# Kernel tuning notes

Measured on AMD Instinct MI355X. Metric: run time of the kernel, lower is better.

The kernel has to match this reference:

```python
import jax, jax.numpy as jnp
import numpy as np

DIM_H = 128
HEADS = 8
HEAD_DIM = DIM_H // HEADS
N_NODES = 40000
N_EDGES = 640000
BN_EPS = 1e-5


def setup_inputs() -> dict:
    key = jax.random.key(0)
    ks = jax.random.split(key, 16)
    s = 0.05
    x = jax.random.normal(ks[0], (N_NODES, DIM_H), dtype=jnp.float32)
    edge_index = jax.random.randint(ks[1], (2, N_EDGES), 0, N_NODES, dtype=jnp.int64)
    p = lambda k, shp: jax.random.normal(k, shp, dtype=jnp.float32) * s
    return {
        "x": x,
        "edge_index": edge_index,
        "Wk": p(ks[2], (DIM_H, DIM_H)), "bk": p(ks[3], (DIM_H,)),
        "Wv": p(ks[4], (DIM_H, DIM_H)), "bv": p(ks[5], (DIM_H,)),
        "Wo": p(ks[6], (DIM_H, DIM_H)), "bo": p(ks[7], (DIM_H,)),
        "bn1_g": jnp.ones((DIM_H,), jnp.float32), "bn1_b": jnp.zeros((DIM_H,), jnp.float32),
        "W1": p(ks[8], (2 * DIM_H, DIM_H)), "b1": p(ks[9], (2 * DIM_H,)),
        "W2": p(ks[10], (DIM_H, 2 * DIM_H)), "b2": p(ks[11], (DIM_H,)),
        "bn2_g": jnp.ones((DIM_H,), jnp.float32), "bn2_b": jnp.zeros((DIM_H,), jnp.float32),
    }


def _batchnorm(h, gamma, beta):
    # BatchNorm1d in training mode: per-feature batch mean / biased var over nodes
    mu = jnp.mean(h, axis=0)
    var = jnp.mean((h - mu) ** 2, axis=0)
    return (h - mu) * jax.lax.rsqrt(var + BN_EPS) * gamma + beta


def _sparse_attn(x, edge_index, Wk, bk, Wv, bv, Wo, bo):
    N = x.shape[0]
    src, dst = edge_index[0], edge_index[1]
    K = (x @ Wk.T + bk).reshape(N, HEADS, HEAD_DIM)
    V = (x @ Wv.T + bv).reshape(N, HEADS, HEAD_DIM)
    Q = x.reshape(N, HEADS, HEAD_DIM)  # query is raw h (no projection)
    # per-edge scores [E, H]
    scores = jnp.sum(K[src] * Q[dst], axis=-1) / np.sqrt(HEAD_DIM).astype(np.float32)
    # segment softmax over destination nodes (pyg_softmax)
    m = jax.ops.segment_max(scores, dst, num_segments=N)
    e = jnp.exp(scores - m[dst])
    denom = jax.ops.segment_sum(e, dst, num_segments=N)
    attn = e / (denom[dst] + 1e-16)  # [E, H]
    messages = V[src] * attn[:, :, None]  # [E, H, D]
    out = jax.ops.segment_sum(messages, dst, num_segments=N)  # [N, H, D]
    return out.reshape(N, DIM_H) @ Wo.T + bo


def reference(x, edge_index, Wk, bk, Wv, bv, Wo, bo, bn1_g, bn1_b,
              W1, b1, W2, b2, bn2_g, bn2_b):
    h_attn = _sparse_attn(x, edge_index, Wk, bk, Wv, bv, Wo, bo)
    h = _batchnorm(x + h_attn, bn1_g, bn1_b)
    ff = jax.nn.relu(h @ W1.T + b1) @ W2.T + b2
    h = _batchnorm(h + ff, bn2_g, bn2_b)
    return h
```

## Files before the change

kernel.cpp:

```cpp
#include <hip/hip_runtime.h>

#define DIM 128
#define NSHARD 8

typedef __attribute__((ext_vector_type(2))) float f32x2;
typedef __attribute__((ext_vector_type(4))) _Float16 half4;
typedef __attribute__((ext_vector_type(8))) _Float16 half8;
typedef __attribute__((ext_vector_type(4))) float f32x4;

#define HP 136
#define UP 264

__device__ __forceinline__ unsigned char to_fp8(float v) {
  return (unsigned char)(__builtin_amdgcn_cvt_pk_fp8_f32(v, v, 0, false) & 0xff);
}

__global__ __launch_bounds__(256) void conv_wall(const float* __restrict__ Wk,
    const float* __restrict__ Wv, const float* __restrict__ Wo,
    const float* __restrict__ W1, const float* __restrict__ W2,
    _Float16* __restrict__ Wkh, _Float16* __restrict__ Wvh,
    _Float16* __restrict__ Woh, _Float16* __restrict__ W1h,
    _Float16* __restrict__ W2h, int* __restrict__ cnt, float* __restrict__ stats,
    int N) {
  int i = blockIdx.x * 256 + threadIdx.x;
  int nth = gridDim.x * 256;
  if (i < 16384) Wkh[i] = (_Float16)Wk[i];
  else if (i < 32768) Wvh[i - 16384] = (_Float16)Wv[i - 16384];
  else if (i < 49152) Woh[i - 32768] = (_Float16)Wo[i - 32768];
  else if (i < 81920) W1h[i - 49152] = (_Float16)W1[i - 49152];
  else if (i < 114688) W2h[i - 81920] = (_Float16)W2[i - 81920];
  for (int j = i; j < N * NSHARD; j += nth) cnt[j] = 0;
  if (i < 512) stats[i] = 0.f;
}

__global__ __launch_bounds__(256) void hist_rank(const int* __restrict__ ei,
    int* __restrict__ cnt, int* __restrict__ rank, int N, int E) {
  int e = blockIdx.x * 256 + threadIdx.x;
  if (e < E) rank[e] = atomicAdd(&cnt[(e & (NSHARD - 1)) * N + ei[E + e]], 1);
}

__global__ __launch_bounds__(256) void scanA(const int* __restrict__ cnt,
    int* __restrict__ rs, int* __restrict__ bsum, int N) {
  __shared__ int s[256];
  int t = threadIdx.x;
  int i = blockIdx.x * 256 + t;
  int v = 0;
  if (i < N)
#pragma unroll
    for (int sh = 0; sh < NSHARD; sh++) v += cnt[sh * N + i];
  s[t] = v;
  __syncthreads();
  for (int off = 1; off < 256; off <<= 1) {
    int add = (t >= off) ? s[t - off] : 0;
    __syncthreads();
    s[t] += add;
    __syncthreads();
  }
  if (i < N) rs[i] = s[t] - v;
  if (t == 255) bsum[blockIdx.x] = s[t];
}

__global__ __launch_bounds__(256) void scanBC(int* __restrict__ rs,
    const int* __restrict__ bsum, const int* __restrict__ cnt,
    int* __restrict__ rs_shard, int nblk, int N, int E) {
  __shared__ int s[256];
  __shared__ int ex[256];
  int t = threadIdx.x;
  int v = (t < nblk) ? bsum[t] : 0;
  s[t] = v;
  __syncthreads();
  for (int off = 1; off < 256; off <<= 1) {
    int add = (t >= off) ? s[t - off] : 0;
    __syncthreads();
    s[t] += add;
    __syncthreads();
  }
  ex[t] = s[t] - v;
  __syncthreads();
  int boff = ex[blockIdx.x];
  int i = blockIdx.x * 256 + t;
  if (i < N) {
    int b = rs[i] + boff;
    rs[i] = b;
#pragma unroll
    for (int sh = 0; sh < NSHARD; sh++) {
      rs_shard[sh * N + i] = b;
      b += cnt[sh * N + i];
    }
  }
  if (i == 0) rs[N] = E;
}

__global__ __launch_bounds__(256) void scatter_kv(const int* __restrict__ ei,
    const int* __restrict__ rs_shard, const int* __restrict__ rank,
    int* __restrict__ esrc, const float* __restrict__ x,
    const _Float16* __restrict__ Wkh, const float* __restrict__ bk,
    const _Float16* __restrict__ Wvh, const float* __restrict__ bv,
    unsigned char* __restrict__ KV8, int kvb, int N, int E) {
  __shared__ _Float16 xs[64 * HP];
  int tid = threadIdx.x;
  if ((int)blockIdx.x >= kvb) {
    int e = ((int)blockIdx.x - kvb) * 256 + tid;
    if (e < E)
      esrc[rs_shard[(e & (NSHARD - 1)) * N + ei[E + e]] + rank[e]] = ei[e];
    return;
  }
  int base = blockIdx.x * 64;
  int lane = tid & 63, w = tid >> 6;
  int l15 = lane & 15, quad = lane >> 4;

  for (int i = tid; i < 64 * 32; i += 256) {
    int m = i >> 5, c4 = i & 31;
    float4 tv = ((const float4*)x)[(size_t)(base + m) * 32 + c4];
    half4 hv;
    hv.x = (_Float16)tv.x; hv.y = (_Float16)tv.y;
    hv.z = (_Float16)tv.z; hv.w = (_Float16)tv.w;
    *(half4*)&xs[m * HP + c4 * 4] = hv;
  }
  __syncthreads();

  half8 afr[4][4];
#pragma unroll
  for (int mt = 0; mt < 4; mt++)
#pragma unroll
    for (int ks = 0; ks < 4; ks++)
      afr[mt][ks] = *(const half8*)&xs[(mt * 16 + l15) * HP + ks * 32 + quad * 8];

  const _Float16* W = (w < 2) ? Wkh : Wvh;
  const float* bias = (w < 2) ? bk : bv;
  int voff = (w < 2) ? 0 : 4;
  int c0 = (w & 1) * 64;

#pragma unroll
  for (int nt = 0; nt < 4; nt++) {
    int f = c0 + nt * 16 + l15;
    half8 bfr[4];
#pragma unroll
    for (int ks = 0; ks < 4; ks++)
      bfr[ks] = *(const half8*)&W[(size_t)f * 128 + ks * 32 + quad * 8];
    f32x4 acc[4];
#pragma unroll
    for (int mt = 0; mt < 4; mt++) acc[mt] = (f32x4){0.f, 0.f, 0.f, 0.f};
#pragma unroll
    for (int ks = 0; ks < 4; ks++)
#pragma unroll
      for (int mt = 0; mt < 4; mt++)
        acc[mt] = __builtin_amdgcn_mfma_f32_16x16x32_f16(afr[mt][ks], bfr[ks],
                                                          acc[mt], 0, 0, 0);
    float bb = bias[f];
    int fo = (f >> 2) * 8 + (f & 3) + voff;
#pragma unroll
    for (int mt = 0; mt < 4; mt++)
#pragma unroll
      for (int r = 0; r < 4; r++)
        KV8[(size_t)(base + mt * 16 + quad * 4 + r) * 256 + fo] =
            to_fp8(acc[mt][r] + bb);
  }
}

__global__ __launch_bounds__(256) void attn_agg(const unsigned char* __restrict__ KV8,
    const float* __restrict__ x, const int* __restrict__ rs,
    const int* __restrict__ esrc, _Float16* __restrict__ attn16, int N) {
  int wave = threadIdx.x >> 6, lane = threadIdx.x & 63;
  int n = blockIdx.x * 4 + wave;
  if (n >= N) return;
  int l = lane & 31, s = lane >> 5;
  float4 q = *(const float4*)&x[(size_t)n * DIM + 4 * l];
  int beg = rs[n], end = rs[n + 1];
  float a0 = 0.f, a1 = 0.f, a2 = 0.f, a3 = 0.f, dloc = 0.f;
  for (int e = beg + s; e < end; e += 8) {
    bool hh[4];
    int ss[4];
#pragma unroll
    for (int u = 0; u < 4; u++) hh[u] = (e + 2 * u) < end;
    ss[0] = esrc[e];
#pragma unroll
    for (int u = 1; u < 4; u++) ss[u] = hh[u] ? esrc[e + 2 * u] : ss[0];
    uint2 kv[4];
#pragma unroll
    for (int u = 0; u < 4; u++)
      kv[u] = *(const uint2*)&KV8[(size_t)ss[u] * 256 + 8 * l];
    float p[4];
#pragma unroll
    for (int u = 0; u < 4; u++) {
      f32x2 k01 = __builtin_amdgcn_cvt_pk_f32_fp8(kv[u].x, false);
      f32x2 k23 = __builtin_amdgcn_cvt_pk_f32_fp8(kv[u].x, true);
      p[u] = k01[0] * q.x + k01[1] * q.y + k23[0] * q.z + k23[1] * q.w;
    }
#pragma unroll
    for (int u = 0; u < 4; u++) p[u] += __shfl_xor(p[u], 1);
#pragma unroll
    for (int u = 0; u < 4; u++) p[u] += __shfl_xor(p[u], 2);
#pragma unroll
    for (int u = 0; u < 4; u++) {
      float ev = hh[u] ? __expf(p[u] * 0.25f) : 0.f;
      dloc += ev;
      f32x2 v01 = __builtin_amdgcn_cvt_pk_f32_fp8(kv[u].y, false);
      f32x2 v23 = __builtin_amdgcn_cvt_pk_f32_fp8(kv[u].y, true);
      a0 += ev * v01[0];
      a1 += ev * v01[1];
      a2 += ev * v23[0];
      a3 += ev * v23[1];
    }
  }
  dloc += __shfl_xor(dloc, 32);
  a0 += __shfl_xor(a0, 32);
  a1 += __shfl_xor(a1, 32);
  a2 += __shfl_xor(a2, 32);
  a3 += __shfl_xor(a3, 32);
  if (s == 0) {
    float inv = 1.0f / (dloc + 1e-16f);
    half4 o;
    o.x = (_Float16)(a0 * inv);
    o.y = (_Float16)(a1 * inv);
    o.z = (_Float16)(a2 * inv);
    o.w = (_Float16)(a3 * inv);
    *(half4*)&attn16[(size_t)n * DIM + 4 * l] = o;
  }
}

__global__ __launch_bounds__(256) void o_proj_mfma(const _Float16* __restrict__ attn16,
    const float* __restrict__ x, const _Float16* __restrict__ Woh,
    const float* __restrict__ bo, _Float16* __restrict__ t16,
    float* __restrict__ stats, int N) {
  __shared__ _Float16 as16[64 * HP];
  int tid = threadIdx.x;
  int base = blockIdx.x * 64;
  int lane = tid & 63, w = tid >> 6;
  int l15 = lane & 15, quad = lane >> 4;

  for (int i = tid; i < 64 * 16; i += 256) {
    int m = i >> 4, c8 = i & 15;
    *(half8*)&as16[m * HP + c8 * 8] =
        ((const half8*)attn16)[(size_t)(base + m) * 16 + c8];
  }
  __syncthreads();

  half8 afr[4][4];
#pragma unroll
  for (int mt = 0; mt < 4; mt++)
#pragma unroll
    for (int ks = 0; ks < 4; ks++)
      afr[mt][ks] = *(const half8*)&as16[(mt * 16 + l15) * HP + ks * 32 + quad * 8];

  int c0 = w * 32;
  f32x4 acc[4][2];
#pragma unroll
  for (int mt = 0; mt < 4; mt++)
#pragma unroll
    for (int nt = 0; nt < 2; nt++) acc[mt][nt] = (f32x4){0.f, 0.f, 0.f, 0.f};
#pragma unroll
  for (int ks = 0; ks < 4; ks++) {
    half8 b[2];
#pragma unroll
    for (int nt = 0; nt < 2; nt++)
      b[nt] = *(const half8*)&Woh[(size_t)(c0 + nt * 16 + l15) * 128 + ks * 32 +
                                  quad * 8];
#pragma unroll
    for (int mt = 0; mt < 4; mt++)
#pragma unroll
      for (int nt = 0; nt < 2; nt++)
        acc[mt][nt] =
            __builtin_amdgcn_mfma_f32_16x16x32_f16(afr[mt][ks], b[nt], acc[mt][nt], 0, 0, 0);
  }

#pragma unroll
  for (int nt = 0; nt < 2; nt++) {
    int f = c0 + nt * 16 + l15;
    float bb = bo[f];
    float s = 0.f, q = 0.f;
#pragma unroll
    for (int mt = 0; mt < 4; mt++) {
#pragma unroll
      for (int r = 0; r < 4; r++) {
        int row = mt * 16 + quad * 4 + r;
        float tv = acc[mt][nt][r] + bb + x[(size_t)(base + row) * DIM + f];
        t16[(size_t)(base + row) * DIM + f] = (_Float16)tv;
        s += tv;
        q += tv * tv;
      }
    }
    s += __shfl_xor(s, 16);
    s += __shfl_xor(s, 32);
    q += __shfl_xor(q, 16);
    q += __shfl_xor(q, 32);
    if (quad == 0) {
      atomicAdd(&stats[f], s);
      atomicAdd(&stats[128 + f], q);
    }
  }
}

__global__ __launch_bounds__(256) void ffn_mfma(const _Float16* __restrict__ t16,
    const float* __restrict__ stats1, const float* __restrict__ g1,
    const float* __restrict__ bb1, const _Float16* __restrict__ W1h,
    const float* __restrict__ b1, const _Float16* __restrict__ W2h,
    const float* __restrict__ b2, _Float16* __restrict__ z16,
    float* __restrict__ stats2, float invN, int N) {
  __shared__ _Float16 hs[64 * HP];
  __shared__ _Float16 us[64 * UP];
  __shared__ float cf[256];
  int tid = threadIdx.x;
  int base = blockIdx.x * 64;
  int lane = tid & 63, w = tid >> 6;
  int l15 = lane & 15, quad = lane >> 4;

  if (tid < 128) {
    float mu = stats1[tid] * invN;
    float var = stats1[128 + tid] * invN - mu * mu;
    float a = rsqrtf(var + 1e-5f) * g1[tid];
    cf[tid] = a;
    cf[128 + tid] = bb1[tid] - mu * a;
  }
  __syncthreads();

  for (int i = tid; i < 64 * 16; i += 256) {
    int m = i >> 4, c8 = i & 15;
    half8 tv = ((const half8*)t16)[(size_t)(base + m) * 16 + c8];
    half8 hv;
#pragma unroll
    for (int j = 0; j < 8; j++) {
      int f = c8 * 8 + j;
      hv[j] = (_Float16)((float)tv[j] * cf[f] + cf[128 + f]);
    }
    *(half8*)&hs[m * HP + c8 * 8] = hv;
  }
  __syncthreads();

  int n0 = w * 64;
  half8 afr[4][4];
#pragma unroll
  for (int mt = 0; mt < 4; mt++)
#pragma unroll
    for (int ks = 0; ks < 4; ks++)
      afr[mt][ks] = *(const half8*)&hs[(mt * 16 + l15) * HP + ks * 32 + quad * 8];

#pragma unroll
  for (int nt = 0; nt < 4; nt++) {
    int n = n0 + nt * 16 + l15;
    half8 bfr[4];
#pragma unroll
    for (int ks = 0; ks < 4; ks++)
      bfr[ks] = *(const half8*)&W1h[(size_t)n * 128 + ks * 32 + quad * 8];
    f32x4 acc[4];
#pragma unroll
    for (int mt = 0; mt < 4; mt++) acc[mt] = (f32x4){0.f, 0.f, 0.f, 0.f};
#pragma unroll
    for (int ks = 0; ks < 4; ks++)
#pragma unroll
      for (int mt = 0; mt < 4; mt++)
        acc[mt] = __builtin_amdgcn_mfma_f32_16x16x32_f16(afr[mt][ks], bfr[ks],
                                                          acc[mt], 0, 0, 0);
    float bias = b1[n];
#pragma unroll
    for (int mt = 0; mt < 4; mt++)
#pragma unroll
      for (int r = 0; r < 4; r++)
        us[(mt * 16 + quad * 4 + r) * UP + n] =
            (_Float16)fmaxf(acc[mt][r] + bias, 0.f);
  }
  __syncthreads();

  int n2 = w * 32;
  f32x4 acc2[4][2];
#pragma unroll
  for (int mt = 0; mt < 4; mt++)
#pragma unroll
    for (int nt = 0; nt < 2; nt++) acc2[mt][nt] = (f32x4){0.f, 0.f, 0.f, 0.f};
  for (int ks = 0; ks < 8; ks++) {
    half8 a[4], b[2];
#pragma unroll
    for (int mt = 0; mt < 4; mt++)
      a[mt] = *(const half8*)&us[(mt * 16 + l15) * UP + ks * 32 + quad * 8];
#pragma unroll
    for (int nt = 0; nt < 2; nt++)
      b[nt] = *(const half8*)&W2h[(size_t)(n2 + nt * 16 + l15) * 256 + ks * 32 +
                                  quad * 8];
#pragma unroll
    for (int mt = 0; mt < 4; mt++)
#pragma unroll
      for (int nt = 0; nt < 2; nt++)
        acc2[mt][nt] =
            __builtin_amdgcn_mfma_f32_16x16x32_f16(a[mt], b[nt], acc2[mt][nt], 0, 0, 0);
  }

#pragma unroll
  for (int nt = 0; nt < 2; nt++) {
    int f = n2 + nt * 16 + l15;
    float bz = b2[f];
    float s = 0.f, q = 0.f;
#pragma unroll
    for (int mt = 0; mt < 4; mt++) {
#pragma unroll
      for (int r = 0; r < 4; r++) {
        int row = mt * 16 + quad * 4 + r;
        float hv = (float)hs[row * HP + f];
        float zv = hv + acc2[mt][nt][r] + bz;
        z16[(size_t)(base + row) * DIM + f] = (_Float16)zv;
        s += zv;
        q += zv * zv;
      }
    }
    s += __shfl_xor(s, 16);
    s += __shfl_xor(s, 32);
    q += __shfl_xor(q, 16);
    q += __shfl_xor(q, 32);
    if (quad == 0) {
      atomicAdd(&stats2[f], s);
      atomicAdd(&stats2[128 + f], q);
    }
  }
}

__global__ __launch_bounds__(256) void final_apply(const _Float16* __restrict__ z16,
    const float* __restrict__ stats2, const float* __restrict__ g2,
    const float* __restrict__ bb2, float* __restrict__ out, float invN,
    int total8) {
  __shared__ float cf[256];
  int tid = threadIdx.x;
  if (tid < 128) {
    float mu = stats2[tid] * invN;
    float var = stats2[128 + tid] * invN - mu * mu;
    float a = rsqrtf(var + 1e-5f) * g2[tid];
    cf[tid] = a;
    cf[128 + tid] = bb2[tid] - mu * a;
  }
  __syncthreads();
  int i = blockIdx.x * 256 + tid;
  if (i >= total8) return;
  int f0 = (i * 8) & 127;
  half8 zv = ((const half8*)z16)[i];
  float4 o1, o2;
  o1.x = (float)zv[0] * cf[f0 + 0] + cf[128 + f0 + 0];
  o1.y = (float)zv[1] * cf[f0 + 1] + cf[128 + f0 + 1];
  o1.z = (float)zv[2] * cf[f0 + 2] + cf[128 + f0 + 2];
  o1.w = (float)zv[3] * cf[f0 + 3] + cf[128 + f0 + 3];
  o2.x = (float)zv[4] * cf[f0 + 4] + cf[128 + f0 + 4];
  o2.y = (float)zv[5] * cf[f0 + 5] + cf[128 + f0 + 5];
  o2.z = (float)zv[6] * cf[f0 + 6] + cf[128 + f0 + 6];
  o2.w = (float)zv[7] * cf[f0 + 7] + cf[128 + f0 + 7];
  ((float4*)out)[2 * i] = o1;
  ((float4*)out)[2 * i + 1] = o2;
}

extern "C" void kernel_launch(void* const* d_in, const int* in_sizes, int n_in,
                              void* d_out, int out_size, void* d_ws, size_t ws_size,
                              hipStream_t stream) {
  const float* x = (const float*)d_in[0];
  const int* ei = (const int*)d_in[1];
  const float* Wk = (const float*)d_in[2];
  const float* bk = (const float*)d_in[3];
  const float* Wv = (const float*)d_in[4];
  const float* bv = (const float*)d_in[5];
  const float* Wo = (const float*)d_in[6];
  const float* bo = (const float*)d_in[7];
  const float* bn1_g = (const float*)d_in[8];
  const float* bn1_b = (const float*)d_in[9];
  const float* W1 = (const float*)d_in[10];
  const float* b1 = (const float*)d_in[11];
  const float* W2 = (const float*)d_in[12];
  const float* b2 = (const float*)d_in[13];
  const float* bn2_g = (const float*)d_in[14];
  const float* bn2_b = (const float*)d_in[15];
  float* out = (float*)d_out;

  int N = in_sizes[0] / DIM;
  int E = in_sizes[1] / 2;

  unsigned char* KV8 = (unsigned char*)d_ws;
  _Float16* attn16 = (_Float16*)(KV8 + (size_t)N * 256);
  _Float16* t16 = attn16 + (size_t)N * DIM;
  _Float16* z16 = t16 + (size_t)N * DIM;
  _Float16* W1h = z16 + (size_t)N * DIM;
  _Float16* W2h = W1h + 32768;
  _Float16* Wkh = W2h + 32768;
  _Float16* Wvh = Wkh + 16384;
  _Float16* Woh = Wvh + 16384;
  float* stats = (float*)(Woh + 16384);
  int* cnt = (int*)(stats + 512);
  int* rs = cnt + (size_t)N * NSHARD;
  int* rs_shard = rs + N + 1;
  int* rank = rs_shard + (size_t)N * NSHARD;
  int* esrc = rank + E;
  int* bsum = esrc + E;

  int nblk = (N + 255) / 256;
  int kvb = N / 64;
  int sblk = (E + 255) / 256;
  float invN = 1.0f / N;
  float* stats2 = stats + 256;

  conv_wall<<<512, 256, 0, stream>>>(Wk, Wv, Wo, W1, W2, Wkh, Wvh, Woh, W1h,
                                     W2h, cnt, stats, N);
  hist_rank<<<sblk, 256, 0, stream>>>(ei, cnt, rank, N, E);
  scanA<<<nblk, 256, 0, stream>>>(cnt, rs, bsum, N);
  scanBC<<<nblk, 256, 0, stream>>>(rs, bsum, cnt, rs_shard, nblk, N, E);
  scatter_kv<<<kvb + sblk, 256, 0, stream>>>(ei, rs_shard, rank, esrc, x, Wkh,
                                             bk, Wvh, bv, KV8, kvb, N, E);
  attn_agg<<<(N + 3) / 4, 256, 0, stream>>>(KV8, x, rs, esrc, attn16, N);
  o_proj_mfma<<<kvb, 256, 0, stream>>>(attn16, x, Woh, bo, t16, stats, N);
  ffn_mfma<<<kvb, 256, 0, stream>>>(t16, stats, bn1_g, bn1_b, W1h, b1, W2h, b2,
                                    z16, stats2, invN, N);
  final_apply<<<((N * DIM / 8) + 255) / 256, 256, 0, stream>>>(
      z16, stats2, bn2_g, bn2_b, out, invN, N * DIM / 8);
}
```

Before: 240.2 us.

## Fuse attention aggregation into O-projection and vectorize MFMA epilogue stores

Merges the edge-aggregation kernel with the output projection, so each block aggregates its 64 nodes into shared memory and feeds them straight to the MFMA, removing the attn16 round trip through global memory and one launch. It also swaps the MFMA operand order so each lane holds four consecutive output features, which allows packed fp8, half4 and float4 stores and loads in the K/V, FFN and O-projection epilogues. Outputs are staged through LDS for coalesced writes. The cost is fewer waves doing the gather (one wave handles 16 nodes serially, with 625 blocks), which may reduce parallelism for latency-bound gathers.

```diff
diff --git a/kernel.cpp b/kernel.cpp
--- a/kernel.cpp
+++ b/kernel.cpp
@@ -10,10 +10,6 @@
 
 #define HP 136
 #define UP 264
-
-__device__ __forceinline__ unsigned char to_fp8(float v) {
-  return (unsigned char)(__builtin_amdgcn_cvt_pk_fp8_f32(v, v, 0, false) & 0xff);
-}
 
 __global__ __launch_bounds__(256) void conv_wall(const float* __restrict__ Wk,
     const float* __restrict__ Wv, const float* __restrict__ Wo,
@@ -133,11 +129,11 @@
 
 #pragma unroll
   for (int nt = 0; nt < 4; nt++) {
-    int f = c0 + nt * 16 + l15;
+    int fl = c0 + nt * 16 + l15;
     half8 bfr[4];
 #pragma unroll
     for (int ks = 0; ks < 4; ks++)
-      bfr[ks] = *(const half8*)&W[(size_t)f * 128 + ks * 32 + quad * 8];
+      bfr[ks] = *(const half8*)&W[(size_t)fl * 128 + ks * 32 + quad * 8];
     f32x4 acc[4];
 #pragma unroll
     for (int mt = 0; mt < 4; mt++) acc[mt] = (f32x4){0.f, 0.f, 0.f, 0.f};
@@ -145,103 +141,98 @@
     for (int ks = 0; ks < 4; ks++)
 #pragma unroll
       for (int mt = 0; mt < 4; mt++)
-        acc[mt] = __builtin_amdgcn_mfma_f32_16x16x32_f16(afr[mt][ks], bfr[ks],
+        acc[mt] = __builtin_amdgcn_mfma_f32_16x16x32_f16(bfr[ks], afr[mt][ks],
                                                           acc[mt], 0, 0, 0);
-    float bb = bias[f];
-    int fo = (f >> 2) * 8 + (f & 3) + voff;
-#pragma unroll
-    for (int mt = 0; mt < 4; mt++)
-#pragma unroll
-      for (int r = 0; r < 4; r++)
-        KV8[(size_t)(base + mt * 16 + quad * 4 + r) * 256 + fo] =
-            to_fp8(acc[mt][r] + bb);
-  }
-}
-
-__global__ __launch_bounds__(256) void attn_agg(const unsigned char* __restrict__ KV8,
-    const float* __restrict__ x, const int* __restrict__ rs,
-    const int* __restrict__ esrc, _Float16* __restrict__ attn16, int N) {
-  int wave = threadIdx.x >> 6, lane = threadIdx.x & 63;
-  int n = blockIdx.x * 4 + wave;
-  if (n >= N) return;
-  int l = lane & 31, s = lane >> 5;
-  float4 q = *(const float4*)&x[(size_t)n * DIM + 4 * l];
-  int beg = rs[n], end = rs[n + 1];
-  float a0 = 0.f, a1 = 0.f, a2 = 0.f, a3 = 0.f, dloc = 0.f;
-  for (int e = beg + s; e < end; e += 8) {
-    bool hh[4];
-    int ss[4];
-#pragma unroll
-    for (int u = 0; u < 4; u++) hh[u] = (e + 2 * u) < end;
-    ss[0] = esrc[e];
-#pragma unroll
-    for (int u = 1; u < 4; u++) ss[u] = hh[u] ? esrc[e + 2 * u] : ss[0];
-    uint2 kv[4];
-#pragma unroll
-    for (int u = 0; u < 4; u++)
-      kv[u] = *(const uint2*)&KV8[(size_t)ss[u] * 256 + 8 * l];
-    float p[4];
-#pragma unroll
-    for (int u = 0; u < 4; u++) {
-      f32x2 k01 = __builtin_amdgcn_cvt_pk_f32_fp8(kv[u].x, false);
-      f32x2 k23 = __builtin_amdgcn_cvt_pk_f32_fp8(kv[u].x, true);
-      p[u] = k01[0] * q.x + k01[1] * q.y + k23[0] * q.z + k23[1] * q.w;
-    }
-#pragma unroll
-    for (int u = 0; u < 4; u++) p[u] += __shfl_xor(p[u], 1);
-#pragma unroll
-    for (int u = 0; u < 4; u++) p[u] += __shfl_xor(p[u], 2);
-#pragma unroll
-    for (int u = 0; u < 4; u++) {
-      float ev = hh[u] ? __expf(p[u] * 0.25f) : 0.f;
-      dloc += ev;
-      f32x2 v01 = __builtin_amdgcn_cvt_pk_f32_fp8(kv[u].y, false);
-      f32x2 v23 = __builtin_amdgcn_cvt_pk_f32_fp8(kv[u].y, true);
-      a0 += ev * v01[0];
-      a1 += ev * v01[1];
-      a2 += ev * v23[0];
-      a3 += ev * v23[1];
-    }
-  }
-  dloc += __shfl_xor(dloc, 32);
-  a0 += __shfl_xor(a0, 32);
-  a1 += __shfl_xor(a1, 32);
-  a2 += __shfl_xor(a2, 32);
-  a3 += __shfl_xor(a3, 32);
-  if (s == 0) {
-    float inv = 1.0f / (dloc + 1e-16f);
-    half4 o;
-    o.x = (_Float16)(a0 * inv);
-    o.y = (_Float16)(a1 * inv);
-    o.z = (_Float16)(a2 * inv);
-    o.w = (_Float16)(a3 * inv);
-    *(half4*)&attn16[(size_t)n * DIM + 4 * l] = o;
-  }
-}
-
-__global__ __launch_bounds__(256) void o_proj_mfma(const _Float16* __restrict__ attn16,
-    const float* __restrict__ x, const _Float16* __restrict__ Woh,
-    const float* __restrict__ bo, _Float16* __restrict__ t16,
-    float* __restrict__ stats, int N) {
+    int f0 = c0 + nt * 16 + quad * 4;
+    float4 bb4 = *(const float4*)&bias[f0];
+    int off = (f0 >> 2) * 8 + voff;
+#pragma unroll
+    for (int mt = 0; mt < 4; mt++) {
+      int wlo = __builtin_amdgcn_cvt_pk_fp8_f32(acc[mt][0] + bb4.x,
+                                                acc[mt][1] + bb4.y, 0, false);
+      int wfull = __builtin_amdgcn_cvt_pk_fp8_f32(acc[mt][2] + bb4.z,
+                                                  acc[mt][3] + bb4.w, wlo, true);
+      *(int*)&KV8[(size_t)(base + mt * 16 + l15) * 256 + off] = wfull;
+    }
+  }
+}
+
+__global__ __launch_bounds__(256) void attn_oproj(
+    const unsigned char* __restrict__ KV8, const float* __restrict__ x,
+    const int* __restrict__ rs, const int* __restrict__ esrc,
+    const _Float16* __restrict__ Woh, const float* __restrict__ bo,
+    _Float16* __restrict__ t16, float* __restrict__ stats, int N) {
   __shared__ _Float16 as16[64 * HP];
   int tid = threadIdx.x;
   int base = blockIdx.x * 64;
   int lane = tid & 63, w = tid >> 6;
+  int l = lane & 31, s = lane >> 5;
+
+  for (int i = 0; i < 16; i++) {
+    int n = base + w * 16 + i;
+    float4 q = *(const float4*)&x[(size_t)n * DIM + 4 * l];
+    int beg = rs[n], end = rs[n + 1];
+    float a0 = 0.f, a1 = 0.f, a2 = 0.f, a3 = 0.f, dloc = 0.f;
+    for (int e = beg + s; e < end; e += 8) {
+      bool hh[4];
+      int ss[4];
+#pragma unroll
+      for (int u = 0; u < 4; u++) hh[u] = (e + 2 * u) < end;
+      ss[0] = esrc[e];
+#pragma unroll
+      for (int u = 1; u < 4; u++) ss[u] = hh[u] ? esrc[e + 2 * u] : ss[0];
+      uint2 kv[4];
+#pragma unroll
+      for (int u = 0; u < 4; u++)
+        kv[u] = *(const uint2*)&KV8[(size_t)ss[u] * 256 + 8 * l];
+      float p[4];
+#pragma unroll
+      for (int u = 0; u < 4; u++) {
+        f32x2 k01 = __builtin_amdgcn_cvt_pk_f32_fp8(kv[u].x, false);
+        f32x2 k23 = __builtin_amdgcn_cvt_pk_f32_fp8(kv[u].x, true);
+        p[u] = k01[0] * q.x + k01[1] * q.y + k23[0] * q.z + k23[1] * q.w;
+      }
+#pragma unroll
+      for (int u = 0; u < 4; u++) p[u] += __shfl_xor(p[u], 1);
+#pragma unroll
+      for (int u = 0; u < 4; u++) p[u] += __shfl_xor(p[u], 2);
+#pragma unroll
+      for (int u = 0; u < 4; u++) {
+        float ev = hh[u] ? __expf(p[u] * 0.25f) : 0.f;
+        dloc += ev;
+        f32x2 v01 = __builtin_amdgcn_cvt_pk_f32_fp8(kv[u].y, false);
+        f32x2 v23 = __builtin_amdgcn_cvt_pk_f32_fp8(kv[u].y, true);
+        a0 += ev * v01[0];
+        a1 += ev * v01[1];
+        a2 += ev * v23[0];
+        a3 += ev * v23[1];
+      }
+    }
+    dloc += __shfl_xor(dloc, 32);
+    a0 += __shfl_xor(a0, 32);
+    a1 += __shfl_xor(a1, 32);
+    a2 += __shfl_xor(a2, 32);
+    a3 += __shfl_xor(a3, 32);
+    if (s == 0) {
+      float inv = 1.0f / (dloc + 1e-16f);
+      half4 o;
+      o.x = (_Float16)(a0 * inv);
+      o.y = (_Float16)(a1 * inv);
+      o.z = (_Float16)(a2 * inv);
+      o.w = (_Float16)(a3 * inv);
+      *(half4*)&as16[(w * 16 + i) * HP + 4 * l] = o;
+    }
+  }
+  __syncthreads();
+
   int l15 = lane & 15, quad = lane >> 4;
-
-  for (int i = tid; i < 64 * 16; i += 256) {
-    int m = i >> 4, c8 = i & 15;
-    *(half8*)&as16[m * HP + c8 * 8] =
-        ((const half8*)attn16)[(size_t)(base + m) * 16 + c8];
-  }
-  __syncthreads();
-
   half8 afr[4][4];
 #pragma unroll
   for (int mt = 0; mt < 4; mt++)
 #pragma unroll
     for (int ks = 0; ks < 4; ks++)
       afr[mt][ks] = *(const half8*)&as16[(mt * 16 + l15) * HP + ks * 32 + quad * 8];
+  __syncthreads();
 
   int c0 = w * 32;
   f32x4 acc[4][2];
@@ -260,34 +251,57 @@
     for (int mt = 0; mt < 4; mt++)
 #pragma unroll
       for (int nt = 0; nt < 2; nt++)
-        acc[mt][nt] =
-            __builtin_amdgcn_mfma_f32_16x16x32_f16(afr[mt][ks], b[nt], acc[mt][nt], 0, 0, 0);
-  }
-
+        acc[mt][nt] = __builtin_amdgcn_mfma_f32_16x16x32_f16(
+            b[nt], afr[mt][ks], acc[mt][nt], 0, 0, 0);
+  }
+
+  float fs[2][4], fq[2][4];
+#pragma unroll
+  for (int nt = 0; nt < 2; nt++)
+#pragma unroll
+    for (int j = 0; j < 4; j++) { fs[nt][j] = 0.f; fq[nt][j] = 0.f; }
 #pragma unroll
   for (int nt = 0; nt < 2; nt++) {
-    int f = c0 + nt * 16 + l15;
-    float bb = bo[f];
-    float s = 0.f, q = 0.f;
+    int f0 = c0 + nt * 16 + quad * 4;
+    float4 bb4 = *(const float4*)&bo[f0];
 #pragma unroll
     for (int mt = 0; mt < 4; mt++) {
-#pragma unroll
-      for (int r = 0; r < 4; r++) {
-        int row = mt * 16 + quad * 4 + r;
-        float tv = acc[mt][nt][r] + bb + x[(size_t)(base + row) * DIM + f];
-        t16[(size_t)(base + row) * DIM + f] = (_Float16)tv;
-        s += tv;
-        q += tv * tv;
+      int row = mt * 16 + l15;
+      float4 xv = *(const float4*)&x[(size_t)(base + row) * DIM + f0];
+      float t0 = acc[mt][nt][0] + bb4.x + xv.x;
+      float t1 = acc[mt][nt][1] + bb4.y + xv.y;
+      float t2 = acc[mt][nt][2] + bb4.z + xv.z;
+      float t3 = acc[mt][nt][3] + bb4.w + xv.w;
+      half4 hv;
+      hv.x = (_Float16)t0; hv.y = (_Float16)t1;
+      hv.z = (_Float16)t2; hv.w = (_Float16)t3;
+      *(half4*)&as16[row * HP + f0] = hv;
+      fs[nt][0] += t0; fq[nt][0] += t0 * t0;
+      fs[nt][1] += t1; fq[nt][1] += t1 * t1;
+      fs[nt][2] += t2; fq[nt][2] += t2 * t2;
+      fs[nt][3] += t3; fq[nt][3] += t3 * t3;
+    }
+  }
+#pragma unroll
+  for (int nt = 0; nt < 2; nt++)
+#pragma unroll
+    for (int j = 0; j < 4; j++) {
+      float sv = fs[nt][j], qv = fq[nt][j];
+      sv += __shfl_xor(sv, 1); qv += __shfl_xor(qv, 1);
+      sv += __shfl_xor(sv, 2); qv += __shfl_xor(qv, 2);
+      sv += __shfl_xor(sv, 4); qv += __shfl_xor(qv, 4);
+      sv += __shfl_xor(sv, 8); qv += __shfl_xor(qv, 8);
+      if (l15 == 0) {
+        int f = c0 + nt * 16 + quad * 4 + j;
+        atomicAdd(&stats[f], sv);
+        atomicAdd(&stats[128 + f], qv);
       }
     }
-    s += __shfl_xor(s, 16);
-    s += __shfl_xor(s, 32);
-    q += __shfl_xor(q, 16);
-    q += __shfl_xor(q, 32);
-    if (quad == 0) {
-      atomicAdd(&stats[f], s);
-      atomicAdd(&stats[128 + f], q);
-    }
+  __syncthreads();
+
+  for (int i2 = tid; i2 < 64 * 16; i2 += 256) {
+    int m = i2 >> 4, c8 = i2 & 15;
+    ((half8*)t16)[(size_t)(base + m) * 16 + c8] = *(half8*)&as16[m * HP + c8 * 8];
   }
 }
 
@@ -337,11 +351,11 @@
 
 #pragma unroll
   for (int nt = 0; nt < 4; nt++) {
-    int n = n0 + nt * 16 + l15;
+    int nl = n0 + nt * 16 + l15;
     half8 bfr[4];
 #pragma unroll
     for (int ks = 0; ks < 4; ks++)
-      bfr[ks] = *(const half8*)&W1h[(size_t)n * 128 + ks * 32 + quad * 8];
+      bfr[ks] = *(const half8*)&W1h[(size_t)nl * 128 + ks * 32 + quad * 8];
     f32x4 acc[4];
 #pragma unroll
     for (int mt = 0; mt < 4; mt++) acc[mt] = (f32x4){0.f, 0.f, 0.f, 0.f};
@@ -349,15 +363,19 @@
     for (int ks = 0; ks < 4; ks++)
 #pragma unroll
       for (int mt = 0; mt < 4; mt++)
-        acc[mt] = __builtin_amdgcn_mfma_f32_16x16x32_f16(afr[mt][ks], bfr[ks],
+        acc[mt] = __builtin_amdgcn_mfma_f32_16x16x32_f16(bfr[ks], afr[mt][ks],
                                                           acc[mt], 0, 0, 0);
-    float bias = b1[n];
-#pragma unroll
-    for (int mt = 0; mt < 4; mt++)
-#pragma unroll
-      for (int r = 0; r < 4; r++)
-        us[(mt * 16 + quad * 4 + r) * UP + n] =
-            (_Float16)fmaxf(acc[mt][r] + bias, 0.f);
+    int u0 = n0 + nt * 16 + quad * 4;
+    float4 bu4 = *(const float4*)&b1[u0];
+#pragma unroll
+    for (int mt = 0; mt < 4; mt++) {
+      half4 uv;
+      uv.x = (_Float16)fmaxf(acc[mt][0] + bu4.x, 0.f);
+      uv.y = (_Float16)fmaxf(acc[mt][1] + bu4.y, 0.f);
+      uv.z = (_Float16)fmaxf(acc[mt][2] + bu4.z, 0.f);
+      uv.w = (_Float16)fmaxf(acc[mt][3] + bu4.w, 0.f);
+      *(half4*)&us[(mt * 16 + l15) * UP + u0] = uv;
+    }
   }
   __syncthreads();
 
@@ -380,35 +398,57 @@
     for (int mt = 0; mt < 4; mt++)
 #pragma unroll
       for (int nt = 0; nt < 2; nt++)
-        acc2[mt][nt] =
-            __builtin_amdgcn_mfma_f32_16x16x32_f16(a[mt], b[nt], acc2[mt][nt], 0, 0, 0);
-  }
-
+        acc2[mt][nt] = __builtin_amdgcn_mfma_f32_16x16x32_f16(
+            b[nt], a[mt], acc2[mt][nt], 0, 0, 0);
+  }
+
+  float fs[2][4], fq[2][4];
+#pragma unroll
+  for (int nt = 0; nt < 2; nt++)
+#pragma unroll
+    for (int j = 0; j < 4; j++) { fs[nt][j] = 0.f; fq[nt][j] = 0.f; }
 #pragma unroll
   for (int nt = 0; nt < 2; nt++) {
-    int f = n2 + nt * 16 + l15;
-    float bz = b2[f];
-    float s = 0.f, q = 0.f;
+    int f0 = n2 + nt * 16 + quad * 4;
+    float4 bz4 = *(const float4*)&b2[f0];
 #pragma unroll
     for (int mt = 0; mt < 4; mt++) {
-#pragma unroll
-      for (int r = 0; r < 4; r++) {
-        int row = mt * 16 + quad * 4 + r;
-        float hv = (float)hs[row * HP + f];
-        float zv = hv + acc2[mt][nt][r] + bz;
-        z16[(size_t)(base + row) * DIM + f] = (_Float16)zv;
-        s += zv;
-        q += zv * zv;
+      int row = mt * 16 + l15;
+      half4 hv = *(const half4*)&hs[row * HP + f0];
+      float z0 = (float)hv.x + acc2[mt][nt][0] + bz4.x;
+      float z1 = (float)hv.y + acc2[mt][nt][1] + bz4.y;
+      float z2 = (float)hv.z + acc2[mt][nt][2] + bz4.z;
+      float z3 = (float)hv.w + acc2[mt][nt][3] + bz4.w;
+      half4 zv;
+      zv.x = (_Float16)z0; zv.y = (_Float16)z1;
+      zv.z = (_Float16)z2; zv.w = (_Float16)z3;
+      *(half4*)&hs[row * HP + f0] = zv;
+      fs[nt][0] += z0; fq[nt][0] += z0 * z0;
+      fs[nt][1] += z1; fq[nt][1] += z1 * z1;
+      fs[nt][2] += z2; fq[nt][2] += z2 * z2;
+      fs[nt][3] += z3; fq[nt][3] += z3 * z3;
+    }
+  }
+#pragma unroll
+  for (int nt = 0; nt < 2; nt++)
+#pragma unroll
+    for (int j = 0; j < 4; j++) {
+      float sv = fs[nt][j], qv = fq[nt][j];
+      sv += __shfl_xor(sv, 1); qv += __shfl_xor(qv, 1);
+      sv += __shfl_xor(sv, 2); qv += __shfl_xor(qv, 2);
+      sv += __shfl_xor(sv, 4); qv += __shfl_xor(qv, 4);
+      sv += __shfl_xor(sv, 8); qv += __shfl_xor(qv, 8);
+      if (l15 == 0) {
+        int f = n2 + nt * 16 + quad * 4 + j;
+        atomicAdd(&stats2[f], sv);
+        atomicAdd(&stats2[128 + f], qv);
       }
     }
-    s += __shfl_xor(s, 16);
-    s += __shfl_xor(s, 32);
-    q += __shfl_xor(q, 16);
-    q += __shfl_xor(q, 32);
-    if (quad == 0) {
-      atomicAdd(&stats2[f], s);
-      atomicAdd(&stats2[128 + f], q);
-    }
+  __syncthreads();
+
+  for (int i = tid; i < 64 * 16; i += 256) {
+    int m = i >> 4, c8 = i & 15;
+    ((half8*)z16)[(size_t)(base + m) * 16 + c8] = *(half8*)&hs[m * HP + c8 * 8];
   }
 }
 
@@ -468,8 +508,7 @@
   int E = in_sizes[1] / 2;
 
   unsigned char* KV8 = (unsigned char*)d_ws;
-  _Float16* attn16 = (_Float16*)(KV8 + (size_t)N * 256);
-  _Float16* t16 = attn16 + (size_t)N * DIM;
+  _Float16* t16 = (_Float16*)(KV8 + (size_t)N * 256);
   _Float16* z16 = t16 + (size_t)N * DIM;
   _Float16* W1h = z16 + (size_t)N * DIM;
   _Float16* W2h = W1h + 32768;
@@ -497,8 +536,7 @@
   scanBC<<<nblk, 256, 0, stream>>>(rs, bsum, cnt, rs_shard, nblk, N, E);
   scatter_kv<<<kvb + sblk, 256, 0, stream>>>(ei, rs_shard, rank, esrc, x, Wkh,
                                              bk, Wvh, bv, KV8, kvb, N, E);
-  attn_agg<<<(N + 3) / 4, 256, 0, stream>>>(KV8, x, rs, esrc, attn16, N);
-  o_proj_mfma<<<kvb, 256, 0, stream>>>(attn16, x, Woh, bo, t16, stats, N);
+  attn_oproj<<<kvb, 256, 0, stream>>>(KV8, x, rs, esrc, Woh, bo, t16, stats, N);
   ffn_mfma<<<kvb, 256, 0, stream>>>(t16, stats, bn1_g, bn1_b, W1h, b1, W2h, b2,
                                     z16, stats2, invN, N);
   final_apply<<<((N * DIM / 8) + 255) / 256, 256, 0, stream>>>(
```

Result: slower. 346.9 us (+44.4%).
